# Kernel optimization log

Measured on AMD Instinct MI355X. Metric: run time of the kernel, lower is better.

## Reference

```python
import jax, jax.numpy as jnp
import numpy as np

N = 50000    # num genes (nodes)
E = 500000   # edges per edge type
T = 2        # edge types
L = 2        # gnn layers
H = 4        # attention heads
D = 64       # per-head channels (hidden // heads)
HID = 256    # hidden channels
PRE_IN = 1024
OUT = 64
EPS = 1e-5
SLOPE = 0.2  # PyG GATv2 leaky_relu negative slope


def _layer_norm(x, g, b):
    mu = x.mean(-1, keepdims=True)
    v = x.var(-1, keepdims=True)
    return (x - mu) / jnp.sqrt(v + EPS) * g + b


def _seg_softmax(score, seg, n):
    m = jax.ops.segment_max(score, seg, num_segments=n)
    ex = jnp.exp(score - m[seg])
    den = jax.ops.segment_sum(ex, seg, num_segments=n)
    return ex / (den[seg] + 1e-16)


def _gatv2_projected(x, src, dst, Wl, Wr, att, bias, Wp, bp):
    # GATv2Conv (share_weights=False, concat heads) followed by Linear projection
    n = x.shape[0]
    xl = (x @ Wl).reshape(n, H, D)
    xr = (x @ Wr).reshape(n, H, D)
    hs = xl[src]                                   # [E,H,D] messages from source
    e = jax.nn.leaky_relu(hs + xr[dst], SLOPE)     # [E,H,D]
    score = jnp.einsum('ehd,hd->eh', e, att)       # [E,H]
    alpha = _seg_softmax(score, dst, n)            # softmax over in-edges of dst
    out = jax.ops.segment_sum(hs * alpha[:, :, None], dst, num_segments=n)
    out = out.reshape(n, H * D) + bias             # concat heads + conv bias
    return out @ Wp + bp                           # ProjectedGATConv linear


def setup_inputs() -> dict:
    key = jax.random.key(0)
    ks = jax.random.split(key, 20)
    s = 0.05
    return {
        'x': jax.random.normal(ks[0], (N, PRE_IN), dtype=jnp.float32),
        'edge_index_0': jax.random.randint(ks[1], (2, E), 0, N, dtype=jnp.int32),
        'edge_index_1': jax.random.randint(ks[2], (2, E), 0, N, dtype=jnp.int32),
        'pre_W0': jax.random.normal(ks[3], (PRE_IN, HID)) * s,
        'pre_b0': jnp.zeros((HID,)),
        'pre_g0': jnp.ones((HID,)),
        'pre_be0': jnp.zeros((HID,)),
        'pre_W1': jax.random.normal(ks[4], (HID, HID)) * s,
        'pre_b1': jnp.zeros((HID,)),
        'pre_g1': jnp.ones((HID,)),
        'pre_be1': jnp.zeros((HID,)),
        # HeteroGnn: L layers x T edge types of ProjectedGATConv(GATv2)
        'gat_Wl': jax.random.normal(ks[5], (L, T, HID, H * D)) * s,
        'gat_Wr': jax.random.normal(ks[6], (L, T, HID, H * D)) * s,
        'gat_att': jax.random.normal(ks[7], (L, T, H, D)) * 0.1,
        'gat_bias': jnp.zeros((L, T, H * D)),
        'proj_W': jax.random.normal(ks[8], (L, T, H * D, HID)) * s,
        'proj_b': jnp.zeros((L, T, HID)),
        # prediction head: Linear(HID,HID) + relu + Linear(HID,OUT)
        'head_W0': jax.random.normal(ks[9], (HID, HID)) * s,
        'head_b0': jnp.zeros((HID,)),
        'head_W1': jax.random.normal(ks[10], (HID, OUT)) * s,
        'head_b1': jnp.zeros((OUT,)),
    }


def reference(x, edge_index_0, edge_index_1, pre_W0, pre_b0, pre_g0, pre_be0,
              pre_W1, pre_b1, pre_g1, pre_be1, gat_Wl, gat_Wr, gat_att,
              gat_bias, proj_W, proj_b, head_W0, head_b0, head_W1, head_b1):
    loop = jnp.arange(N, dtype=edge_index_0.dtype)  # add_self_loops=True
    edges = [(jnp.concatenate([ei[0], loop]), jnp.concatenate([ei[1], loop]))
             for ei in (edge_index_0, edge_index_1)]
    # preprocessor MLP
    h = jax.nn.relu(_layer_norm(x @ pre_W0 + pre_b0, pre_g0, pre_be0))
    h = jax.nn.relu(_layer_norm(h @ pre_W1 + pre_b1, pre_g1, pre_be1))
    # hetero GAT stack, HeteroConv aggr='sum'
    for l in range(L):
        acc = jnp.zeros((N, HID), dtype=h.dtype)
        for t in range(T):
            src, dst = edges[t]
            acc = acc + _gatv2_projected(h, src, dst, gat_Wl[l, t], gat_Wr[l, t],
                                         gat_att[l, t], gat_bias[l, t],
                                         proj_W[l, t], proj_b[l, t])
        h = jax.nn.relu(acc)
    # prediction head
    h2 = jax.nn.relu(h @ head_W0 + head_b0)
    return h2 @ head_W1 + head_b1
```

## Files before the change

kernel.cpp:

```cpp
#include <hip/hip_runtime.h>
#include <hip/hip_bf16.h>
#include <math.h>

#define N_NODES 50000
#define MP      50048
#define E_EDGES 500000
#define EPRIME  (E_EDGES + N_NODES)
#define HID     256
#define PRE_IN  1024
#define OUT_DIM 64
#define NHEAD   4
#define DHEAD   64
#define LAYERS  2
#define NTYPES  2

#define SCAN_NBLK 49
#define NPAD      (SCAN_NBLK * 1024)

typedef __attribute__((ext_vector_type(8))) short short8v;
typedef __attribute__((ext_vector_type(4))) float f32x4;
typedef _Float16 h2v __attribute__((ext_vector_type(2)));
typedef _Float16 h8v __attribute__((ext_vector_type(8)));

__device__ __forceinline__ ushort f2bf(float f) {
  uint u = __float_as_uint(f);
  u += 0x7FFF + ((u >> 16) & 1);
  return (ushort)(u >> 16);
}
__device__ __forceinline__ float bf2f(ushort u) {
  return __uint_as_float(((uint)u) << 16);
}

template<bool AF32>
__global__ __launch_bounds__(256) void gemm_k(
    const void* __restrict__ Ap,
    const ushort* __restrict__ Bt,
    int K, int M, int N,
    float*  __restrict__ Cf,
    ushort* __restrict__ Cb,
    const float* __restrict__ bias,
    const float* __restrict__ bias2,
    int do_relu, int out_f16)
{
  __shared__ ushort As[128 * 32];
  __shared__ ushort Bs[64 * 32];
  const int tid = threadIdx.x;
  const int l   = tid & 63;
  const int w   = tid >> 6;
  const int wm  = w & 1;
  const int wn  = w >> 1;
  const int bm  = blockIdx.y * 128;
  const int bn  = blockIdx.x * 64;

  f32x4 acc[4][2];
#pragma unroll
  for (int m = 0; m < 4; m++)
#pragma unroll
    for (int n = 0; n < 2; n++) acc[m][n] = (f32x4){0.f, 0.f, 0.f, 0.f};

  const int srow  = l >> 2;
  const int sslot = l & 3;

  const int brow  = tid >> 2;
  const int bslot = tid & 3;
  const int bkc   = bslot ^ ((brow >> 1) & 3);

  for (int k0 = 0; k0 < K; k0 += 32) {
    {
      const ushort* gb = Bt + (size_t)(bn + brow) * K + k0 + bkc * 8;
      __builtin_amdgcn_global_load_lds(
          (const __attribute__((address_space(1))) uint*)gb,
          (__attribute__((address_space(3))) uint*)((char*)Bs + tid * 16), 16, 0, 0);
    }
#pragma unroll
    for (int i = 0; i < 2; i++) {
      const int row = w * 32 + i * 16 + srow;
      const int kc  = sslot ^ ((row >> 1) & 3);
      const uint off = (uint)row * 64 + (uint)sslot * 16;
      if constexpr (AF32) {
        const float* ga = (const float*)Ap + (size_t)(bm + row) * K + k0 + kc * 8;
        float4 v0 = make_float4(0.f, 0.f, 0.f, 0.f);
        float4 v1 = make_float4(0.f, 0.f, 0.f, 0.f);
        if (bm + row < M) {
          v0 = *reinterpret_cast<const float4*>(ga);
          v1 = *reinterpret_cast<const float4*>(ga + 4);
        }
        short8v s;
        s[0] = (short)f2bf(v0.x); s[1] = (short)f2bf(v0.y);
        s[2] = (short)f2bf(v0.z); s[3] = (short)f2bf(v0.w);
        s[4] = (short)f2bf(v1.x); s[5] = (short)f2bf(v1.y);
        s[6] = (short)f2bf(v1.z); s[7] = (short)f2bf(v1.w);
        *reinterpret_cast<short8v*>((char*)As + off) = s;
      } else {
        const ushort* ga = (const ushort*)Ap + (size_t)(bm + row) * K + k0 + kc * 8;
        __builtin_amdgcn_global_load_lds(
            (const __attribute__((address_space(1))) uint*)ga,
            (__attribute__((address_space(3))) uint*)((char*)As + off), 16, 0, 0);
      }
    }
    __syncthreads();

    short8v a[4], b[2];
#pragma unroll
    for (int m = 0; m < 4; m++) {
      const int row = wm * 64 + m * 16 + (l & 15);
      const int kc  = (l >> 4) ^ ((row >> 1) & 3);
      a[m] = *(const short8v*)((const char*)As + row * 64 + kc * 16);
    }
#pragma unroll
    for (int n = 0; n < 2; n++) {
      const int row = wn * 32 + n * 16 + (l & 15);
      const int kc  = (l >> 4) ^ ((row >> 1) & 3);
      b[n] = *(const short8v*)((const char*)Bs + row * 64 + kc * 16);
    }
#pragma unroll
    for (int m = 0; m < 4; m++)
#pragma unroll
      for (int n = 0; n < 2; n++)
        acc[m][n] = __builtin_amdgcn_mfma_f32_16x16x32_bf16(a[m], b[n], acc[m][n], 0, 0, 0);
    __syncthreads();
  }

  const int crow0 = bm + wm * 64 + (l >> 4) * 4;
  const int ccol0 = bn + wn * 32 + (l & 15);
#pragma unroll
  for (int m = 0; m < 4; m++) {
#pragma unroll
    for (int j = 0; j < 4; j++) {
      const int grow = crow0 + m * 16 + j;
      if (grow < M) {
#pragma unroll
        for (int n = 0; n < 2; n++) {
          const int gcol = ccol0 + n * 16;
          if (gcol < N) {
            float v = acc[m][n][j];
            if (bias)  v += bias[gcol];
            if (bias2) v += bias2[gcol];
            if (do_relu) v = fmaxf(v, 0.f);
            if (Cf) Cf[(size_t)grow * N + gcol] = v;
            else if (out_f16) {
              _Float16 hv = (_Float16)v;
              Cb[(size_t)grow * N + gcol] = *(ushort*)&hv;
            } else {
              Cb[(size_t)grow * N + gcol] = f2bf(v);
            }
          }
        }
      }
    }
  }
}

__global__ void ln_relu(const float* __restrict__ in, ushort* __restrict__ out,
                        const float* __restrict__ g, const float* __restrict__ be, int n)
{
  int gid = blockIdx.x * blockDim.x + threadIdx.x;
  int row = gid >> 6;
  int lane = threadIdx.x & 63;
  if (row >= n) return;
  float4 v = *reinterpret_cast<const float4*>(in + (size_t)row * HID + lane * 4);
  float s = v.x + v.y + v.z + v.w;
  float ss = v.x * v.x + v.y * v.y + v.z * v.z + v.w * v.w;
#pragma unroll
  for (int o = 1; o < 64; o <<= 1) { s += __shfl_xor(s, o); ss += __shfl_xor(ss, o); }
  float mu = s * (1.f / 256.f);
  float var = ss * (1.f / 256.f) - mu * mu;
  float inv = rsqrtf(var + 1e-5f);
  float4 gg = *reinterpret_cast<const float4*>(g + lane * 4);
  float4 bb = *reinterpret_cast<const float4*>(be + lane * 4);
  ushort4 o4;
  o4.x = f2bf(fmaxf((v.x - mu) * inv * gg.x + bb.x, 0.f));
  o4.y = f2bf(fmaxf((v.y - mu) * inv * gg.y + bb.y, 0.f));
  o4.z = f2bf(fmaxf((v.z - mu) * inv * gg.z + bb.z, 0.f));
  o4.w = f2bf(fmaxf((v.w - mu) * inv * gg.w + bb.w, 0.f));
  *reinterpret_cast<ushort4*>(out + (size_t)row * HID + lane * 4) = o4;
}

__global__ void csr_count2(const int* __restrict__ ei0, const int* __restrict__ ei1,
                           int* __restrict__ cnt0, int* __restrict__ cnt1)
{
  int e = blockIdx.x * blockDim.x + threadIdx.x;
  if (e >= 2 * EPRIME) return;
  int type = e >= EPRIME;
  int i = type ? e - EPRIME : e;
  const int* ei = type ? ei1 : ei0;
  int* cnt = type ? cnt1 : cnt0;
  int d = (i < E_EDGES) ? ei[E_EDGES + i] : (i - E_EDGES);
  atomicAdd(&cnt[d], 1);
}

__global__ __launch_bounds__(256) void scan_p1(const int* __restrict__ cnt0,
                                               const int* __restrict__ cnt1,
                                               int* __restrict__ bsums)
{
  int type = blockIdx.x >= SCAN_NBLK;
  int blk = type ? blockIdx.x - SCAN_NBLK : blockIdx.x;
  const int* cnt = type ? cnt1 : cnt0;
  int4 v = reinterpret_cast<const int4*>(cnt)[blk * 256 + threadIdx.x];
  int s = v.x + v.y + v.z + v.w;
#pragma unroll
  for (int o = 1; o < 64; o <<= 1) s += __shfl_xor(s, o);
  __shared__ int wt[4];
  if ((threadIdx.x & 63) == 0) wt[threadIdx.x >> 6] = s;
  __syncthreads();
  if (threadIdx.x == 0) bsums[blockIdx.x] = wt[0] + wt[1] + wt[2] + wt[3];
}

__global__ void scan_p2(const int* __restrict__ bsums, int* __restrict__ boffs,
                        int* __restrict__ offs0, int* __restrict__ offs1)
{
  int t = threadIdx.x;
  if (t < 2) {
    int run = 0;
    for (int i = 0; i < SCAN_NBLK; i++) {
      boffs[t * SCAN_NBLK + i] = run;
      run += bsums[t * SCAN_NBLK + i];
    }
  }
  if (t == 2) offs0[N_NODES] = EPRIME;
  if (t == 3) offs1[N_NODES] = EPRIME;
}

__global__ __launch_bounds__(256) void scan_p3(
    const int* __restrict__ cnt0, const int* __restrict__ cnt1,
    const int* __restrict__ boffs,
    int* __restrict__ offs0, int* __restrict__ cur0,
    int* __restrict__ offs1, int* __restrict__ cur1)
{
  int type = blockIdx.x >= SCAN_NBLK;
  int blk = type ? blockIdx.x - SCAN_NBLK : blockIdx.x;
  const int* cnt = type ? cnt1 : cnt0;
  int* offs = type ? offs1 : offs0;
  int* cur  = type ? cur1 : cur0;
  const int tid = threadIdx.x, lane = tid & 63, wv = tid >> 6;
  int4 v = reinterpret_cast<const int4*>(cnt)[blk * 256 + tid];
  int e1 = v.x, e2 = e1 + v.y, e3 = e2 + v.z, T = e3 + v.w;
  int incl = T;
#pragma unroll
  for (int o = 1; o < 64; o <<= 1) {
    int nb = __shfl_up(incl, o);
    if (lane >= o) incl += nb;
  }
  __shared__ int wt[4];
  if (lane == 63) wt[wv] = incl;
  __syncthreads();
  int wexcl = 0;
  for (int i = 0; i < wv; i++) wexcl += wt[i];
  int base = boffs[blockIdx.x] + wexcl + (incl - T);
  int idx = blk * 1024 + tid * 4;
  int4 o4 = make_int4(base, base + e1, base + e2, base + e3);
  if (idx + 3 < N_NODES) {
    reinterpret_cast<int4*>(offs)[idx >> 2] = o4;
    reinterpret_cast<int4*>(cur)[idx >> 2] = o4;
  } else {
    if (idx + 0 < N_NODES) { offs[idx + 0] = o4.x; cur[idx + 0] = o4.x; }
    if (idx + 1 < N_NODES) { offs[idx + 1] = o4.y; cur[idx + 1] = o4.y; }
    if (idx + 2 < N_NODES) { offs[idx + 2] = o4.z; cur[idx + 2] = o4.z; }
    if (idx + 3 < N_NODES) { offs[idx + 3] = o4.w; cur[idx + 3] = o4.w; }
  }
}

__global__ void csr_scatter2(const int* __restrict__ ei0, const int* __restrict__ ei1,
                             int* __restrict__ cur0, int* __restrict__ cur1,
                             int* __restrict__ csr0, int* __restrict__ csr1)
{
  int e = blockIdx.x * blockDim.x + threadIdx.x;
  if (e >= 2 * EPRIME) return;
  int type = e >= EPRIME;
  int i = type ? e - EPRIME : e;
  const int* ei = type ? ei1 : ei0;
  int* cur = type ? cur1 : cur0;
  int* csr = type ? csr1 : csr0;
  int d = (i < E_EDGES) ? ei[E_EDGES + i] : (i - E_EDGES);
  int s = (i < E_EDGES) ? ei[i] : (i - E_EDGES);
  int pos = atomicAdd(&cur[d], 1);
  csr[pos] = s;
}

__global__ void csr_sort2(const int* __restrict__ offs0, int* __restrict__ csr0,
                          const int* __restrict__ offs1, int* __restrict__ csr1)
{
  int d = blockIdx.x * blockDim.x + threadIdx.x;
  if (d >= 2 * N_NODES) return;
  int type = d >= N_NODES;
  int i = type ? d - N_NODES : d;
  const int* offs = type ? offs1 : offs0;
  int* csr = type ? csr1 : csr0;
  int b = offs[i], e = offs[i + 1];
  for (int p = b + 1; p < e; p++) {
    int v = csr[p];
    int j = p - 1;
    while (j >= b && csr[j] > v) { csr[j + 1] = csr[j]; j--; }
    csr[j + 1] = v;
  }
}

#define WSEG0 262144
#define WSEG1 (WSEG0 + 65536)
#define WSEG2 (WSEG1 + 524288)
#define WSEG3 (WSEG2 + 262144)
#define WSEG4 (WSEG3 + 65536)
#define WSEG5 (WSEG4 + 32768)
__global__ void wtrans_all(const float* __restrict__ pre_W0, const float* __restrict__ pre_W1,
                           const float* __restrict__ Wl, const float* __restrict__ Wr,
                           const float* __restrict__ proj_W,
                           const float* __restrict__ head_W0, const float* __restrict__ head_W1,
                           ushort* __restrict__ W0t, ushort* __restrict__ W1t,
                           ushort* __restrict__ WcatT, ushort* __restrict__ projcatT,
                           ushort* __restrict__ hW0t, ushort* __restrict__ hW1t)
{
  int i = blockIdx.x * blockDim.x + threadIdx.x;
  if (i < WSEG0) {
    int nrow = i >> 10, k = i & 1023;
    W0t[i] = f2bf(pre_W0[(size_t)k * 256 + nrow]);
  } else if (i < WSEG1) {
    int j = i - WSEG0;
    int nrow = j >> 8, k = j & 255;
    W1t[j] = f2bf(pre_W1[(size_t)k * 256 + nrow]);
  } else if (i < WSEG2) {
    int j = i - WSEG1;
    int l = j >> 18;
    int rem = j & 262143;
    int c = rem >> 8, k = rem & 255;
    int t = c >> 9, half = (c >> 8) & 1, cc = c & 255;
    const float* W = half ? Wr : Wl;
    WcatT[j] = f2bf(W[(((size_t)l * NTYPES + t) * 256 + k) * 256 + cc]);
  } else if (i < WSEG3) {
    int j = i - WSEG2;
    int l = j >> 17;
    int rem = j & 131071;
    int n = rem >> 9, k = rem & 511;
    int t = k >> 8, kk = k & 255;
    projcatT[j] = f2bf(proj_W[(((size_t)l * NTYPES + t) * 256 + kk) * 256 + n]);
  } else if (i < WSEG4) {
    int j = i - WSEG3;
    int nrow = j >> 8, k = j & 255;
    hW0t[j] = f2bf(head_W0[(size_t)k * 256 + nrow]);
  } else if (i < WSEG5) {
    int j = i - WSEG4;
    int nrow = j >> 8, k = j & 255;
    hW1t[j] = (nrow < OUT_DIM) ? f2bf(head_W1[(size_t)k * OUT_DIM + nrow]) : (ushort)0;
  }
}

__device__ __forceinline__ float dpp8_sum(float p) {
  p += __int_as_float(__builtin_amdgcn_update_dpp(0, __float_as_int(p), 0xB1, 0xF, 0xF, true));
  p += __int_as_float(__builtin_amdgcn_update_dpp(0, __float_as_int(p), 0x4E, 0xF, 0xF, true));
  p += __int_as_float(__builtin_amdgcn_update_dpp(0, __float_as_int(p), 0x141, 0xF, 0xF, true));
  return p;
}

__device__ __forceinline__ h8v leaky8(h8v x) {
  const _Float16 c = (_Float16)0.2f;
  h8v y = x * c;
#if __has_builtin(__builtin_elementwise_max)
  return __builtin_elementwise_max(x, y);
#else
  h8v r;
#pragma unroll
  for (int i = 0; i < 8; i++) r[i] = x[i] > y[i] ? x[i] : y[i];
  return r;
#endif
}

__device__ __forceinline__ float dot8(h8v e, const h2v* a) {
  h2v e0 = {e[0], e[1]}, e1 = {e[2], e[3]}, e2 = {e[4], e[5]}, e3 = {e[6], e[7]};
#if __has_builtin(__builtin_amdgcn_fdot2)
  float s = __builtin_amdgcn_fdot2(e0, a[0], 0.f, false);
  s = __builtin_amdgcn_fdot2(e1, a[1], s, false);
  s = __builtin_amdgcn_fdot2(e2, a[2], s, false);
  s = __builtin_amdgcn_fdot2(e3, a[3], s, false);
  return s;
#else
  float s = 0.f;
#pragma unroll
  for (int i = 0; i < 8; i++) s += (float)e[i] * (float)a[i >> 1][i & 1];
  return s;
#endif
}

__global__ __launch_bounds__(256) void gat_edge3(
    const _Float16* __restrict__ xlr,
    const int* __restrict__ offs0, const int* __restrict__ csr0,
    const int* __restrict__ offs1, const int* __restrict__ csr1,
    const float* __restrict__ att,
    const float* __restrict__ bias,
    ushort* __restrict__ out, int nblk_per_type)
{
  const int type = blockIdx.x >= nblk_per_type;
  const int bid = type ? blockIdx.x - nblk_per_type : blockIdx.x;
  const int wid = (bid * 256 + threadIdx.x) >> 6;
  if (wid >= N_NODES) return;
  const int lane = threadIdx.x & 63;
  const int half = lane >> 5, li = lane & 31;
  const int* offs = type ? offs1 : offs0;
  const int* csr  = type ? csr1 : csr0;
  const int xl_col = type ? 512 : 0;

  const float* ap = att + type * 256 + li * 8;
  h2v a[4];
#pragma unroll
  for (int i = 0; i < 4; i++) {
    a[i][0] = (_Float16)ap[2 * i];
    a[i][1] = (_Float16)ap[2 * i + 1];
  }
  const h8v xr = *reinterpret_cast<const h8v*>(xlr + (size_t)wid * 1024 + xl_col + 256 + li * 8);

  const int beg = offs[wid], end = offs[wid + 1];
  const float L2E = 1.44269504f;
  float m = -1e30f, den = 0.f;
  float acc[8];
#pragma unroll
  for (int i = 0; i < 8; i++) acc[i] = 0.f;

  const int ng = (end - beg + 3) >> 2;
  for (int g = 0; g < ng; g++) {
    const int j0 = beg + 4 * g + half;
    const int j1 = j0 + 2;
    const bool v0 = j0 < end, v1 = j1 < end;
    const int s0 = csr[v0 ? j0 : beg];
    const int s1 = csr[v1 ? j1 : beg];
    const h8v hs0 = *reinterpret_cast<const h8v*>(xlr + (size_t)s0 * 1024 + xl_col + li * 8);
    const h8v hs1 = *reinterpret_cast<const h8v*>(xlr + (size_t)s1 * 1024 + xl_col + li * 8);
    float p0 = dpp8_sum(dot8(leaky8(hs0 + xr), a));
    float p1 = dpp8_sum(dot8(leaky8(hs1 + xr), a));
    if (!v0) p0 = -INFINITY;
    if (!v1) p1 = -INFINITY;
    const float pm = fmaxf(p0, p1);
    if (__any(pm > m + 4.f)) {
      const float nm = fmaxf(m, pm);
      const float so = exp2f((m - nm) * L2E);
      den *= so;
#pragma unroll
      for (int i = 0; i < 8; i++) acc[i] *= so;
      m = nm;
    }
    const float w0 = exp2f((p0 - m) * L2E);
    const float w1 = exp2f((p1 - m) * L2E);
    den += w0 + w1;
#pragma unroll
    for (int i = 0; i < 8; i++) {
      acc[i] = fmaf((float)hs0[i], w0, acc[i]);
      acc[i] = fmaf((float)hs1[i], w1, acc[i]);
    }
  }

  const float mo  = __shfl_xor(m, 32);
  const float dno = __shfl_xor(den, 32);
  const float ms = fmaxf(m, mo);
  const float fa = exp2f((m - ms) * L2E);
  const float fb = exp2f((mo - ms) * L2E);
  const float r = 1.f / (den * fa + dno * fb + 1e-16f);
  float of[8];
#pragma unroll
  for (int i = 0; i < 8; i++)
    of[i] = (acc[i] * fa + __shfl_xor(acc[i], 32) * fb) * r;

  if (half == 0) {
    const float* bp = bias + type * 256 + li * 8;
    uint4 o;
    uint pk[4];
#pragma unroll
    for (int i = 0; i < 4; i++) {
      const uint lo = f2bf(of[2 * i] + bp[2 * i]);
      const uint hi = f2bf(of[2 * i + 1] + bp[2 * i + 1]);
      pk[i] = lo | (hi << 16);
    }
    o.x = pk[0]; o.y = pk[1]; o.z = pk[2]; o.w = pk[3];
    *reinterpret_cast<uint4*>(out + (size_t)wid * 512 + type * 256 + li * 8) = o;
  }
}

extern "C" void kernel_launch(void* const* d_in, const int* in_sizes, int n_in,
                              void* d_out, int out_size, void* d_ws, size_t ws_size,
                              hipStream_t stream)
{
  const float* x        = (const float*)d_in[0];
  const int*   ei0      = (const int*)d_in[1];
  const int*   ei1      = (const int*)d_in[2];
  const float* pre_W0   = (const float*)d_in[3];
  const float* pre_b0   = (const float*)d_in[4];
  const float* pre_g0   = (const float*)d_in[5];
  const float* pre_be0  = (const float*)d_in[6];
  const float* pre_W1   = (const float*)d_in[7];
  const float* pre_b1   = (const float*)d_in[8];
  const float* pre_g1   = (const float*)d_in[9];
  const float* pre_be1  = (const float*)d_in[10];
  const float* gat_Wl   = (const float*)d_in[11];
  const float* gat_Wr   = (const float*)d_in[12];
  const float* gat_att  = (const float*)d_in[13];
  const float* gat_bias = (const float*)d_in[14];
  const float* proj_W   = (const float*)d_in[15];
  const float* proj_b   = (const float*)d_in[16];
  const float* head_W0  = (const float*)d_in[17];
  const float* head_b0  = (const float*)d_in[18];
  const float* head_W1  = (const float*)d_in[19];
  const float* head_b1  = (const float*)d_in[20];
  float* outp = (float*)d_out;

  char* ws = (char*)d_ws;
  ushort* xlr_b = (ushort*)ws; ws += (size_t)MP * 1024 * 2;
  ushort* hb    = (ushort*)ws; ws += (size_t)MP * 256 * 2;
  ushort* outt  = (ushort*)ws; ws += (size_t)MP * 512 * 2;
  float*  tmp   = (float*)outt;
  ushort* hbuf  = (ushort*)outt;
  ushort* W0t      = (ushort*)ws; ws += (size_t)256 * 1024 * 2;
  ushort* W1t      = (ushort*)ws; ws += (size_t)256 * 256 * 2;
  ushort* WcatT    = (ushort*)ws; ws += (size_t)LAYERS * 1024 * 256 * 2;
  ushort* projcatT = (ushort*)ws; ws += (size_t)LAYERS * 256 * 512 * 2;
  ushort* hW0t     = (ushort*)ws; ws += (size_t)256 * 256 * 2;
  ushort* hW1t     = (ushort*)ws; ws += (size_t)128 * 256 * 2;
  int* cnt0  = (int*)ws; ws += (size_t)NPAD * 4;
  int* cnt1  = (int*)ws; ws += (size_t)NPAD * 4;
  int* offs0 = (int*)ws; ws += (size_t)(N_NODES + 4) * 4;
  int* offs1 = (int*)ws; ws += (size_t)(N_NODES + 4) * 4;
  int* cur0  = (int*)ws; ws += (size_t)N_NODES * 4;
  int* cur1  = (int*)ws; ws += (size_t)N_NODES * 4;
  int* bsums = (int*)ws; ws += (size_t)128 * 4;
  int* boffs = (int*)ws; ws += (size_t)128 * 4;
  int* csr0  = (int*)ws; ws += (size_t)EPRIME * 4;
  int* csr1  = (int*)ws; ws += (size_t)EPRIME * 4;

  hipMemsetAsync(cnt0, 0, (size_t)2 * NPAD * 4, stream);
  const int gE2 = (2 * EPRIME + 255) / 256;
  csr_count2<<<gE2, 256, 0, stream>>>(ei0, ei1, cnt0, cnt1);
  scan_p1<<<2 * SCAN_NBLK, 256, 0, stream>>>(cnt0, cnt1, bsums);
  scan_p2<<<1, 64, 0, stream>>>(bsums, boffs, offs0, offs1);
  scan_p3<<<2 * SCAN_NBLK, 256, 0, stream>>>(cnt0, cnt1, boffs, offs0, cur0, offs1, cur1);
  csr_scatter2<<<gE2, 256, 0, stream>>>(ei0, ei1, cur0, cur1, csr0, csr1);
  csr_sort2<<<(2 * N_NODES + 255) / 256, 256, 0, stream>>>(offs0, csr0, offs1, csr1);

  wtrans_all<<<WSEG5 / 256, 256, 0, stream>>>(pre_W0, pre_W1, gat_Wl, gat_Wr, proj_W,
                                              head_W0, head_W1,
                                              W0t, W1t, WcatT, projcatT, hW0t, hW1t);

  const dim3 blk(256);
  const int gy = MP / 128;
  const int gln = (N_NODES * 64 + 255) / 256;

  gemm_k<true><<<dim3(4, gy), blk, 0, stream>>>(x, W0t, 1024, N_NODES, 256,
                                                tmp, nullptr, pre_b0, nullptr, 0, 0);
  ln_relu<<<gln, 256, 0, stream>>>(tmp, hb, pre_g0, pre_be0, N_NODES);
  gemm_k<false><<<dim3(4, gy), blk, 0, stream>>>(hb, W1t, 256, N_NODES, 256,
                                                 tmp, nullptr, pre_b1, nullptr, 0, 0);
  ln_relu<<<gln, 256, 0, stream>>>(tmp, hb, pre_g1, pre_be1, N_NODES);

  for (int l = 0; l < LAYERS; l++) {
    gemm_k<false><<<dim3(16, gy), blk, 0, stream>>>(hb, WcatT + (size_t)l * 1024 * 256,
                                                    256, N_NODES, 1024,
                                                    nullptr, xlr_b, nullptr, nullptr, 0, 1);
    gat_edge3<<<2 * gln, 256, 0, stream>>>(
        (const _Float16*)xlr_b, offs0, csr0, offs1, csr1,
        gat_att  + (size_t)l * NTYPES * NHEAD * DHEAD,
        gat_bias + (size_t)l * NTYPES * HID,
        outt, gln);
    gemm_k<false><<<dim3(4, gy), blk, 0, stream>>>(
        outt, projcatT + (size_t)l * 256 * 512, 512, N_NODES, 256,
        nullptr, hb,
        proj_b + (size_t)(l * NTYPES + 0) * HID,
        proj_b + (size_t)(l * NTYPES + 1) * HID, 1, 0);
  }

  gemm_k<false><<<dim3(4, gy), blk, 0, stream>>>(hb, hW0t, 256, N_NODES, 256,
                                                 nullptr, hbuf, head_b0, nullptr, 1, 0);
  gemm_k<false><<<dim3(1, gy), blk, 0, stream>>>(hbuf, hW1t, 256, N_NODES, OUT_DIM,
                                                 outp, nullptr, head_b1, nullptr, 0, 0);
}
```

Baseline: 868.9 us.

## Pre-cast x to bf16, fuse prep kernels, XCD-swizzle GEMM tiles, prefetch CSR indices

Merges weight transposition, edge counting and a new fp32-to-bf16 cast of x into one prep kernel. This lets the first GEMM load its A operand directly to LDS through global_load_lds instead of converting in registers. The GEMM tile order is remapped so neighbouring tiles land on the same XCD, aiming at better L2 reuse. The GAT edge loop also prefetches the next group's CSR source indices. The cast adds a full extra read and write pass over x in exchange for a faster first GEMM, and the bf16 x reuses the xlr buffer. Rows past N in the padded buffer are now read unguarded.

After: 775.7 us. -10.7%, faster.

```diff
diff --git a/kernel.cpp b/kernel.cpp
--- a/kernel.cpp
+++ b/kernel.cpp
@@ -31,9 +31,8 @@
   return __uint_as_float(((uint)u) << 16);
 }
 
-template<bool AF32>
 __global__ __launch_bounds__(256) void gemm_k(
-    const void* __restrict__ Ap,
+    const ushort* __restrict__ A,
     const ushort* __restrict__ Bt,
     int K, int M, int N,
     float*  __restrict__ Cf,
@@ -49,8 +48,15 @@
   const int w   = tid >> 6;
   const int wm  = w & 1;
   const int wn  = w >> 1;
-  const int bm  = blockIdx.y * 128;
-  const int bn  = blockIdx.x * 64;
+
+  const int nwg  = gridDim.x * gridDim.y;
+  const int orig = blockIdx.y * gridDim.x + blockIdx.x;
+  const int qq   = nwg >> 3, rr = nwg & 7;
+  const int xcd  = orig & 7;
+  const int wgid = ((xcd < rr) ? xcd * (qq + 1) : rr * (qq + 1) + (xcd - rr) * qq)
+                   + (orig >> 3);
+  const int bm = (wgid / gridDim.x) * 128;
+  const int bn = (wgid % gridDim.x) * 64;
 
   f32x4 acc[4][2];
 #pragma unroll
@@ -60,12 +66,22 @@
 
   const int srow  = l >> 2;
   const int sslot = l & 3;
-
+  const int nt    = K >> 5;
+
+  int  arow[2], akc[2];
+  uint aoff[2];
+#pragma unroll
+  for (int i = 0; i < 2; i++) {
+    arow[i] = w * 32 + i * 16 + srow;
+    akc[i]  = sslot ^ ((arow[i] >> 1) & 3);
+    aoff[i] = (uint)arow[i] * 64 + (uint)sslot * 16;
+  }
   const int brow  = tid >> 2;
   const int bslot = tid & 3;
   const int bkc   = bslot ^ ((brow >> 1) & 3);
 
-  for (int k0 = 0; k0 < K; k0 += 32) {
+  for (int t = 0; t < nt; t++) {
+    const int k0 = t << 5;
     {
       const ushort* gb = Bt + (size_t)(bn + brow) * K + k0 + bkc * 8;
       __builtin_amdgcn_global_load_lds(
@@ -74,29 +90,10 @@
     }
 #pragma unroll
     for (int i = 0; i < 2; i++) {
-      const int row = w * 32 + i * 16 + srow;
-      const int kc  = sslot ^ ((row >> 1) & 3);
-      const uint off = (uint)row * 64 + (uint)sslot * 16;
-      if constexpr (AF32) {
-        const float* ga = (const float*)Ap + (size_t)(bm + row) * K + k0 + kc * 8;
-        float4 v0 = make_float4(0.f, 0.f, 0.f, 0.f);
-        float4 v1 = make_float4(0.f, 0.f, 0.f, 0.f);
-        if (bm + row < M) {
-          v0 = *reinterpret_cast<const float4*>(ga);
-          v1 = *reinterpret_cast<const float4*>(ga + 4);
-        }
-        short8v s;
-        s[0] = (short)f2bf(v0.x); s[1] = (short)f2bf(v0.y);
-        s[2] = (short)f2bf(v0.z); s[3] = (short)f2bf(v0.w);
-        s[4] = (short)f2bf(v1.x); s[5] = (short)f2bf(v1.y);
-        s[6] = (short)f2bf(v1.z); s[7] = (short)f2bf(v1.w);
-        *reinterpret_cast<short8v*>((char*)As + off) = s;
-      } else {
-        const ushort* ga = (const ushort*)Ap + (size_t)(bm + row) * K + k0 + kc * 8;
-        __builtin_amdgcn_global_load_lds(
-            (const __attribute__((address_space(1))) uint*)ga,
-            (__attribute__((address_space(3))) uint*)((char*)As + off), 16, 0, 0);
-      }
+      const ushort* ga = A + (size_t)(bm + arow[i]) * K + k0 + akc[i] * 8;
+      __builtin_amdgcn_global_load_lds(
+          (const __attribute__((address_space(1))) uint*)ga,
+          (__attribute__((address_space(3))) uint*)((char*)As + aoff[i]), 16, 0, 0);
     }
     __syncthreads();
 
@@ -176,17 +173,87 @@
   *reinterpret_cast<ushort4*>(out + (size_t)row * HID + lane * 4) = o4;
 }
 
-__global__ void csr_count2(const int* __restrict__ ei0, const int* __restrict__ ei1,
-                           int* __restrict__ cnt0, int* __restrict__ cnt1)
-{
-  int e = blockIdx.x * blockDim.x + threadIdx.x;
-  if (e >= 2 * EPRIME) return;
-  int type = e >= EPRIME;
-  int i = type ? e - EPRIME : e;
-  const int* ei = type ? ei1 : ei0;
-  int* cnt = type ? cnt1 : cnt0;
-  int d = (i < E_EDGES) ? ei[E_EDGES + i] : (i - E_EDGES);
-  atomicAdd(&cnt[d], 1);
+#define WSEG0 262144
+#define WSEG1 (WSEG0 + 65536)
+#define WSEG2 (WSEG1 + 524288)
+#define WSEG3 (WSEG2 + 262144)
+#define WSEG4 (WSEG3 + 65536)
+#define WSEG5 (WSEG4 + 32768)
+#define NWT   (WSEG5 / 256)
+#define NCNT  ((2 * EPRIME + 255) / 256)
+#define NCAST 4096
+#define CAST_UNITS (N_NODES * 1024 / 8)
+
+__global__ void prep_all(const float* __restrict__ pre_W0, const float* __restrict__ pre_W1,
+                         const float* __restrict__ Wl, const float* __restrict__ Wr,
+                         const float* __restrict__ proj_W,
+                         const float* __restrict__ head_W0, const float* __restrict__ head_W1,
+                         ushort* __restrict__ W0t, ushort* __restrict__ W1t,
+                         ushort* __restrict__ WcatT, ushort* __restrict__ projcatT,
+                         ushort* __restrict__ hW0t, ushort* __restrict__ hW1t,
+                         const int* __restrict__ ei0, const int* __restrict__ ei1,
+                         int* __restrict__ cnt0, int* __restrict__ cnt1,
+                         const float* __restrict__ x, ushort* __restrict__ xb)
+{
+  const int bid = blockIdx.x;
+  if (bid < NWT) {
+    int i = bid * 256 + threadIdx.x;
+    if (i < WSEG0) {
+      int nrow = i >> 10, k = i & 1023;
+      W0t[i] = f2bf(pre_W0[(size_t)k * 256 + nrow]);
+    } else if (i < WSEG1) {
+      int j = i - WSEG0;
+      int nrow = j >> 8, k = j & 255;
+      W1t[j] = f2bf(pre_W1[(size_t)k * 256 + nrow]);
+    } else if (i < WSEG2) {
+      int j = i - WSEG1;
+      int l = j >> 18;
+      int rem = j & 262143;
+      int c = rem >> 8, k = rem & 255;
+      int t = c >> 9, half = (c >> 8) & 1, cc = c & 255;
+      const float* W = half ? Wr : Wl;
+      WcatT[j] = f2bf(W[(((size_t)l * NTYPES + t) * 256 + k) * 256 + cc]);
+    } else if (i < WSEG3) {
+      int j = i - WSEG2;
+      int l = j >> 17;
+      int rem = j & 131071;
+      int n = rem >> 9, k = rem & 511;
+      int t = k >> 8, kk = k & 255;
+      projcatT[j] = f2bf(proj_W[(((size_t)l * NTYPES + t) * 256 + kk) * 256 + n]);
+    } else if (i < WSEG4) {
+      int j = i - WSEG3;
+      int nrow = j >> 8, k = j & 255;
+      hW0t[j] = f2bf(head_W0[(size_t)k * 256 + nrow]);
+    } else if (i < WSEG5) {
+      int j = i - WSEG4;
+      int nrow = j >> 8, k = j & 255;
+      hW1t[j] = (nrow < OUT_DIM) ? f2bf(head_W1[(size_t)k * OUT_DIM + nrow]) : (ushort)0;
+    }
+  } else if (bid < NWT + NCNT) {
+    int e = (bid - NWT) * 256 + threadIdx.x;
+    if (e < 2 * EPRIME) {
+      int type = e >= EPRIME;
+      int i = type ? e - EPRIME : e;
+      const int* ei = type ? ei1 : ei0;
+      int* cnt = type ? cnt1 : cnt0;
+      int d = (i < E_EDGES) ? ei[E_EDGES + i] : (i - E_EDGES);
+      atomicAdd(&cnt[d], 1);
+    }
+  } else {
+    const float4* xf = (const float4*)x;
+    short8v* xo = (short8v*)xb;
+    for (size_t i = (size_t)(bid - NWT - NCNT) * 256 + threadIdx.x;
+         i < (size_t)CAST_UNITS; i += (size_t)NCAST * 256) {
+      float4 v0 = xf[2 * i];
+      float4 v1 = xf[2 * i + 1];
+      short8v s;
+      s[0] = (short)f2bf(v0.x); s[1] = (short)f2bf(v0.y);
+      s[2] = (short)f2bf(v0.z); s[3] = (short)f2bf(v0.w);
+      s[4] = (short)f2bf(v1.x); s[5] = (short)f2bf(v1.y);
+      s[6] = (short)f2bf(v1.z); s[7] = (short)f2bf(v1.w);
+      xo[i] = s;
+    }
+  }
 }
 
 __global__ __launch_bounds__(256) void scan_p1(const int* __restrict__ cnt0,
@@ -295,54 +362,6 @@
   }
 }
 
-#define WSEG0 262144
-#define WSEG1 (WSEG0 + 65536)
-#define WSEG2 (WSEG1 + 524288)
-#define WSEG3 (WSEG2 + 262144)
-#define WSEG4 (WSEG3 + 65536)
-#define WSEG5 (WSEG4 + 32768)
-__global__ void wtrans_all(const float* __restrict__ pre_W0, const float* __restrict__ pre_W1,
-                           const float* __restrict__ Wl, const float* __restrict__ Wr,
-                           const float* __restrict__ proj_W,
-                           const float* __restrict__ head_W0, const float* __restrict__ head_W1,
-                           ushort* __restrict__ W0t, ushort* __restrict__ W1t,
-                           ushort* __restrict__ WcatT, ushort* __restrict__ projcatT,
-                           ushort* __restrict__ hW0t, ushort* __restrict__ hW1t)
-{
-  int i = blockIdx.x * blockDim.x + threadIdx.x;
-  if (i < WSEG0) {
-    int nrow = i >> 10, k = i & 1023;
-    W0t[i] = f2bf(pre_W0[(size_t)k * 256 + nrow]);
-  } else if (i < WSEG1) {
-    int j = i - WSEG0;
-    int nrow = j >> 8, k = j & 255;
-    W1t[j] = f2bf(pre_W1[(size_t)k * 256 + nrow]);
-  } else if (i < WSEG2) {
-    int j = i - WSEG1;
-    int l = j >> 18;
-    int rem = j & 262143;
-    int c = rem >> 8, k = rem & 255;
-    int t = c >> 9, half = (c >> 8) & 1, cc = c & 255;
-    const float* W = half ? Wr : Wl;
-    WcatT[j] = f2bf(W[(((size_t)l * NTYPES + t) * 256 + k) * 256 + cc]);
-  } else if (i < WSEG3) {
-    int j = i - WSEG2;
-    int l = j >> 17;
-    int rem = j & 131071;
-    int n = rem >> 9, k = rem & 511;
-    int t = k >> 8, kk = k & 255;
-    projcatT[j] = f2bf(proj_W[(((size_t)l * NTYPES + t) * 256 + kk) * 256 + n]);
-  } else if (i < WSEG4) {
-    int j = i - WSEG3;
-    int nrow = j >> 8, k = j & 255;
-    hW0t[j] = f2bf(head_W0[(size_t)k * 256 + nrow]);
-  } else if (i < WSEG5) {
-    int j = i - WSEG4;
-    int nrow = j >> 8, k = j & 255;
-    hW1t[j] = (nrow < OUT_DIM) ? f2bf(head_W1[(size_t)k * OUT_DIM + nrow]) : (ushort)0;
-  }
-}
-
 __device__ __forceinline__ float dpp8_sum(float p) {
   p += __int_as_float(__builtin_amdgcn_update_dpp(0, __float_as_int(p), 0xB1, 0xF, 0xF, true));
   p += __int_as_float(__builtin_amdgcn_update_dpp(0, __float_as_int(p), 0x4E, 0xF, 0xF, true));
@@ -414,12 +433,14 @@
   for (int i = 0; i < 8; i++) acc[i] = 0.f;
 
   const int ng = (end - beg + 3) >> 2;
+  int j0 = beg + half, j1 = j0 + 2;
+  int s0 = csr[j0 < end ? j0 : beg];
+  int s1 = csr[j1 < end ? j1 : beg];
   for (int g = 0; g < ng; g++) {
-    const int j0 = beg + 4 * g + half;
-    const int j1 = j0 + 2;
     const bool v0 = j0 < end, v1 = j1 < end;
-    const int s0 = csr[v0 ? j0 : beg];
-    const int s1 = csr[v1 ? j1 : beg];
+    const int nj0 = j0 + 4, nj1 = j1 + 4;
+    const int ns0 = csr[nj0 < end ? nj0 : beg];
+    const int ns1 = csr[nj1 < end ? nj1 : beg];
     const h8v hs0 = *reinterpret_cast<const h8v*>(xlr + (size_t)s0 * 1024 + xl_col + li * 8);
     const h8v hs1 = *reinterpret_cast<const h8v*>(xlr + (size_t)s1 * 1024 + xl_col + li * 8);
     float p0 = dpp8_sum(dot8(leaky8(hs0 + xr), a));
@@ -443,6 +464,7 @@
       acc[i] = fmaf((float)hs0[i], w0, acc[i]);
       acc[i] = fmaf((float)hs1[i], w1, acc[i]);
     }
+    j0 = nj0; j1 = nj1; s0 = ns0; s1 = ns1;
   }
 
   const float mo  = __shfl_xor(m, 32);
@@ -500,6 +522,7 @@
 
   char* ws = (char*)d_ws;
   ushort* xlr_b = (ushort*)ws; ws += (size_t)MP * 1024 * 2;
+  ushort* xb    = xlr_b;
   ushort* hb    = (ushort*)ws; ws += (size_t)MP * 256 * 2;
   ushort* outt  = (ushort*)ws; ws += (size_t)MP * 512 * 2;
   float*  tmp   = (float*)outt;
@@ -522,47 +545,47 @@
   int* csr1  = (int*)ws; ws += (size_t)EPRIME * 4;
 
   hipMemsetAsync(cnt0, 0, (size_t)2 * NPAD * 4, stream);
+  prep_all<<<NWT + NCNT + NCAST, 256, 0, stream>>>(
+      pre_W0, pre_W1, gat_Wl, gat_Wr, proj_W, head_W0, head_W1,
+      W0t, W1t, WcatT, projcatT, hW0t, hW1t,
+      ei0, ei1, cnt0, cnt1, x, xb);
+
   const int gE2 = (2 * EPRIME + 255) / 256;
-  csr_count2<<<gE2, 256, 0, stream>>>(ei0, ei1, cnt0, cnt1);
   scan_p1<<<2 * SCAN_NBLK, 256, 0, stream>>>(cnt0, cnt1, bsums);
   scan_p2<<<1, 64, 0, stream>>>(bsums, boffs, offs0, offs1);
   scan_p3<<<2 * SCAN_NBLK, 256, 0, stream>>>(cnt0, cnt1, boffs, offs0, cur0, offs1, cur1);
   csr_scatter2<<<gE2, 256, 0, stream>>>(ei0, ei1, cur0, cur1, csr0, csr1);
   csr_sort2<<<(2 * N_NODES + 255) / 256, 256, 0, stream>>>(offs0, csr0, offs1, csr1);
 
-  wtrans_all<<<WSEG5 / 256, 256, 0, stream>>>(pre_W0, pre_W1, gat_Wl, gat_Wr, proj_W,
-                                              head_W0, head_W1,
-                                              W0t, W1t, WcatT, projcatT, hW0t, hW1t);
-
   const dim3 blk(256);
   const int gy = MP / 128;
   const int gln = (N_NODES * 64 + 255) / 256;
 
-  gemm_k<true><<<dim3(4, gy), blk, 0, stream>>>(x, W0t, 1024, N_NODES, 256,
-                                                tmp, nullptr, pre_b0, nullptr, 0, 0);
+  gemm_k<<<dim3(4, gy), blk, 0, stream>>>(xb, W0t, 1024, N_NODES, 256,
+                                          tmp, nullptr, pre_b0, nullptr, 0, 0);
   ln_relu<<<gln, 256, 0, stream>>>(tmp, hb, pre_g0, pre_be0, N_NODES);
-  gemm_k<false><<<dim3(4, gy), blk, 0, stream>>>(hb, W1t, 256, N_NODES, 256,
-                                                 tmp, nullptr, pre_b1, nullptr, 0, 0);
+  gemm_k<<<dim3(4, gy), blk, 0, stream>>>(hb, W1t, 256, N_NODES, 256,
+                                          tmp, nullptr, pre_b1, nullptr, 0, 0);
   ln_relu<<<gln, 256, 0, stream>>>(tmp, hb, pre_g1, pre_be1, N_NODES);
 
   for (int l = 0; l < LAYERS; l++) {
-    gemm_k<false><<<dim3(16, gy), blk, 0, stream>>>(hb, WcatT + (size_t)l * 1024 * 256,
-                                                    256, N_NODES, 1024,
-                                                    nullptr, xlr_b, nullptr, nullptr, 0, 1);
+    gemm_k<<<dim3(16, gy), blk, 0, stream>>>(hb, WcatT + (size_t)l * 1024 * 256,
+                                             256, N_NODES, 1024,
+                                             nullptr, xlr_b, nullptr, nullptr, 0, 1);
     gat_edge3<<<2 * gln, 256, 0, stream>>>(
         (const _Float16*)xlr_b, offs0, csr0, offs1, csr1,
         gat_att  + (size_t)l * NTYPES * NHEAD * DHEAD,
         gat_bias + (size_t)l * NTYPES * HID,
         outt, gln);
-    gemm_k<false><<<dim3(4, gy), blk, 0, stream>>>(
+    gemm_k<<<dim3(4, gy), blk, 0, stream>>>(
         outt, projcatT + (size_t)l * 256 * 512, 512, N_NODES, 256,
         nullptr, hb,
         proj_b + (size_t)(l * NTYPES + 0) * HID,
         proj_b + (size_t)(l * NTYPES + 1) * HID, 1, 0);
   }
 
-  gemm_k<false><<<dim3(4, gy), blk, 0, stream>>>(hb, hW0t, 256, N_NODES, 256,
-                                                 nullptr, hbuf, head_b0, nullptr, 1, 0);
-  gemm_k<false><<<dim3(1, gy), blk, 0, stream>>>(hbuf, hW1t, 256, N_NODES, OUT_DIM,
-                                                 outp, nullptr, head_b1, nullptr, 0, 0);
-}
+  gemm_k<<<dim3(4, gy), blk, 0, stream>>>(hb, hW0t, 256, N_NODES, 256,
+                                          nullptr, hbuf, head_b0, nullptr, 1, 0);
+  gemm_k<<<dim3(1, gy), blk, 0, stream>>>(hbuf, hW1t, 256, N_NODES, OUT_DIM,
+                                          outp, nullptr, head_b1, nullptr, 0, 0);
+}
```
